# Performance work log

Measured on AMD Instinct MI355X. Metric: run time of the kernel, lower is better.

Reference implementation:

```python
import jax, jax.numpy as jnp
import numpy as np

H = 1024
A = H // 2
B = 32
S = 1024
T = 1024


def setup_inputs() -> dict:
    key = jax.random.key(0)
    ks = jax.random.split(key, 16)
    sc = 0.02
    inp = {
        "hidden": jax.random.normal(ks[0], (1, B, H), jnp.float32),
        "encoder_hiddens": jax.random.normal(ks[1], (S, B, H), jnp.float32),
        "h0_s": jax.random.normal(ks[2], (T, B, H), jnp.float32),
        "ax": jax.random.uniform(ks[3], (B, S, 1), jnp.float32),
        # weights: torch Linear(in,out,bias=False) -> W has shape [out,in], y = x @ W.T
        "W1": jax.random.normal(ks[4], (A, H), jnp.float32) * sc,
        "W2": jax.random.normal(ks[5], (A, H), jnp.float32) * sc,
        "W3": jax.random.normal(ks[6], (A, 1), jnp.float32) * sc,
        "W4": jax.random.normal(ks[7], (1, 3 * A), jnp.float32) * sc,
        "W5": jax.random.normal(ks[8], (A, H), jnp.float32) * sc,
        "W6": jax.random.normal(ks[9], (A, H), jnp.float32) * sc,
        "W7": jax.random.normal(ks[10], (A, H), jnp.float32) * sc,
        "W8": jax.random.normal(ks[11], (1, 3 * A), jnp.float32) * sc,
        "W9": jax.random.normal(ks[12], (H, H), jnp.float32) * sc,
        "W10": jax.random.normal(ks[13], (H, H), jnp.float32) * sc,
        "W11": jax.random.normal(ks[14], (1, 2 * H), jnp.float32) * sc,
    }
    return inp


def reference(hidden, encoder_hiddens, h0_s, ax,
              W1, W2, W3, W4, W5, W6, W7, W8, W9, W10, W11):
    h = hidden[0]  # [B,H], hidden.squeeze(0)

    # ---- encoder (x) attention with coverage, vectorized over S ----
    wx = jnp.einsum('sbh,ah->sba', encoder_hiddens, W1)          # [S,B,A]
    wxy = h @ W2.T                                               # [B,A]
    # Linear3 on ax[:, j] ([B,1]): outer product with W3 column
    wxr = ax[:, :, 0][:, :, None] * W3[:, 0][None, None, :]       # [B,S,A]
    wxr = jnp.transpose(wxr, (1, 0, 2))                           # [S,B,A]
    cat_x = jnp.tanh(jnp.concatenate(
        [wx, jnp.broadcast_to(wxy, (S,) + wxy.shape), wxr], axis=-1))  # [S,B,3A]
    exi = jnp.einsum('sbc,oc->bso', cat_x, W4)                    # [B,S,1]
    axi = jax.nn.softmax(exi, axis=1)                             # [B,S,1]
    cxi = jnp.einsum('bs,sbh->bh', axi[:, :, 0], encoder_hiddens)  # [B,H]
    ax_new = ax + axi

    # ---- decoder-history (t) attention, vectorized over T ----
    wt = jnp.einsum('tbh,ah->tba', h0_s, W5)                      # [T,B,A]
    wtx = cxi @ W6.T                                              # [B,A]
    wty = h @ W7.T                                                # [B,A]
    Tn = h0_s.shape[0]
    cat_t = jnp.tanh(jnp.concatenate(
        [wt,
         jnp.broadcast_to(wtx, (Tn,) + wtx.shape),
         jnp.broadcast_to(wty, (Tn,) + wty.shape)], axis=-1))     # [T,B,3A]
    eti = jnp.einsum('tbc,oc->bto', cat_t, W8)                    # [B,T,1]
    ati = jax.nn.softmax(eti, axis=1)
    cti = jnp.einsum('bt,tbh->bh', ati[:, :, 0], h0_s)            # [B,H]

    # ---- gated fusion ----
    gxi = jnp.tanh(cxi @ W9.T)
    gti = jnp.tanh(cti @ W10.T)
    zi = jax.nn.sigmoid(jnp.concatenate([cxi, cti], axis=1) @ W11.T)  # [B,1]
    ci = zi * gxi + (1.0 - zi) * gti                              # [B,H]
    return ci, ax_new
```

## Files before the change

kernel.cpp:

```cpp
#include <hip/hip_runtime.h>
#include <hip/hip_bf16.h>

#define HH 1024
#define AA 512
#define BB 32
#define SS 1024
#define TN 1024
#define M_ENC (SS*BB)
#define M_TOT ((SS+TN)*BB)
#define NCH 8

#define ABUF 8192

typedef __attribute__((ext_vector_type(8))) short short8;
typedef __attribute__((ext_vector_type(4))) float f4;

union bfu { __hip_bfloat16 h; unsigned short u; };
__device__ __forceinline__ unsigned int f2bu(float x) {
  bfu t; t.h = __float2bfloat16(x); return (unsigned int)t.u;
}
__device__ __forceinline__ unsigned short f2b(float x) {
  bfu t; t.h = __float2bfloat16(x); return t.u;
}
__device__ __forceinline__ float tanh_fast(float x) {
  float e = __expf(2.f * x);
  return 1.f - 2.f / (e + 1.f);
}

__global__ void wprep(const float* __restrict__ W, unsigned short* __restrict__ Wc) {
  const int t = blockIdx.x * 256 + threadIdx.x;
  const int lane = t & 63;
  const int rg = (t >> 6) & 31;
  const int kb = t >> 11;
  const int row = rg * 16 + (lane & 15);
  const int k = kb * 32 + ((lane >> 4) << 3);
  const float* src = W + (size_t)row * HH + k;
  f4 v0 = *(const f4*)(src);
  f4 v1 = *(const f4*)(src + 4);
  short8 o;
  o[0] = f2b(v0[0]); o[1] = f2b(v0[1]); o[2] = f2b(v0[2]); o[3] = f2b(v0[3]);
  o[4] = f2b(v1[0]); o[5] = f2b(v1[1]); o[6] = f2b(v1[2]); o[7] = f2b(v1[3]);
  *(short8*)(Wc + (size_t)t * 8) = o;
}

__global__ void poly_prep(const float* __restrict__ W3, const float* __restrict__ W4,
                          float* __restrict__ C) {
  __shared__ float r1[AA], r3[AA], r5[AA];
  const int a = threadIdx.x;
  const float w = W3[a], u = W4[2 * AA + a];
  const float w2 = w * w;
  r1[a] = u * w;
  r3[a] = u * w * w2;
  r5[a] = u * w * w2 * w2;
  __syncthreads();
  for (int off = 256; off > 0; off >>= 1) {
    if (a < off) { r1[a] += r1[a + off]; r3[a] += r3[a + off]; r5[a] += r5[a + off]; }
    __syncthreads();
  }
  if (a == 0) { C[0] = r1[0]; C[1] = -r3[0] / 3.f; C[2] = r5[0] * (2.f / 15.f); }
}

__global__ __launch_bounds__(512, 4)
void e1_gemm(const float* __restrict__ enc, const float* __restrict__ h0,
             const unsigned short* __restrict__ W1c, const unsigned short* __restrict__ W5c,
             const float* __restrict__ W4, const float* __restrict__ W8,
             float* __restrict__ e1s, float* __restrict__ e1t) {
  const int wg   = blockIdx.x;
  const int tid  = threadIdx.x;
  const int lane = tid & 63;
  const int colg = tid >> 6;
  const int l15  = lane & 15;
  const int lg   = lane >> 4;
  const int koff = (wg & 1) << 3;

  const bool is_enc = (wg * 64) < M_ENC;
  const float* __restrict__ Xg = is_enc ? enc : h0;
  const unsigned short* __restrict__ Wc = is_enc ? W1c : W5c;
  const float* __restrict__ Vg = is_enc ? W4 : W8;
  const int row0 = is_enc ? wg * 64 : wg * 64 - M_ENC;

  __shared__ char lds_raw[2 * ABUF];
  float* lred = (float*)lds_raw;

  f4 acc[4][4];
#pragma unroll
  for (int i = 0; i < 4; ++i)
#pragma unroll
    for (int j = 0; j < 4; ++j) acc[i][j] = (f4){0.f, 0.f, 0.f, 0.f};

  const int arow = tid >> 3;
  const int aq   = tid & 7;
  const float* ap = Xg + (size_t)(row0 + arow) * HH + aq * 4;
  const int slotS = (aq >> 1) ^ ((arow >> 1) & 3);
  const int aDst = arow * 64 + slotS * 16 + (aq & 1) * 8;

  const int aRd = l15 * 64 + ((lg ^ ((l15 >> 1) & 3)) << 4);

  const char* bp = (const char*)Wc + colg * 4096 + lane * 16;

  f4 an0, an1;
  short8 bfr[8];

#define ALOAD(k_) do {                                                        \
    an0 = *(const f4*)(ap + (k_) * 64);                                       \
    an1 = *(const f4*)(ap + (k_) * 64 + 32);                                  \
  } while (0)

#define AWR(bo_) do {                                                         \
    uint2 o0_, o1_;                                                           \
    o0_.x = f2bu(an0[0]) | (f2bu(an0[1]) << 16);                              \
    o0_.y = f2bu(an0[2]) | (f2bu(an0[3]) << 16);                              \
    o1_.x = f2bu(an1[0]) | (f2bu(an1[1]) << 16);                              \
    o1_.y = f2bu(an1[2]) | (f2bu(an1[3]) << 16);                              \
    *(uint2*)(lds_raw + (bo_) + aDst) = o0_;                                  \
    *(uint2*)(lds_raw + (bo_) + 4096 + aDst) = o1_;                           \
  } while (0)

#define BLOAD(kb2_) do {                                                      \
    const char* b_ = bp + (size_t)(kb2_) * 65536;                             \
    _Pragma("unroll")                                                         \
    for (int q_ = 0; q_ < 8; ++q_)                                            \
      bfr[q_] = *(const short8*)(b_ + (q_ >> 2) * 32768 + (q_ & 3) * 1024);   \
  } while (0)

#define COMPUTE(bo_) do {                                                     \
    const char* base_ = lds_raw + (bo_);                                      \
    _Pragma("unroll")                                                         \
    for (int ks_ = 0; ks_ < 2; ++ks_) {                                       \
      __builtin_amdgcn_s_setprio(1);                                          \
      _Pragma("unroll")                                                       \
      for (int rt = 0; rt < 4; ++rt) {                                        \
        short8 af_ = *(const short8*)(base_ + ks_ * 4096 + aRd + rt * 1024);  \
        _Pragma("unroll")                                                     \
        for (int cf = 0; cf < 4; ++cf)                                        \
          acc[rt][cf] = __builtin_amdgcn_mfma_f32_16x16x32_bf16(              \
              af_, bfr[ks_ * 4 + cf], acc[rt][cf], 0, 0, 0);                  \
      }                                                                       \
      __builtin_amdgcn_s_setprio(0);                                          \
    }                                                                         \
  } while (0)

#define SYNCA() do {                                                          \
    __builtin_amdgcn_sched_barrier(0);                                        \
    asm volatile("s_waitcnt lgkmcnt(0)" ::: "memory");                        \
    __builtin_amdgcn_s_barrier();                                             \
    __builtin_amdgcn_sched_barrier(0);                                        \
  } while (0)

  ALOAD(koff);
  AWR(0);
  ALOAD((1 + koff) & 15);
  SYNCA();

#pragma unroll 1
  for (int it = 0; it < 7; ++it) {
    const int kc0 = (2 * it + koff) & 15;
    const int ka2 = (2 * it + 2 + koff) & 15;
    const int kc1 = (2 * it + 1 + koff) & 15;
    const int ka3 = (2 * it + 3 + koff) & 15;
    AWR(ABUF); ALOAD(ka2); BLOAD(kc0); COMPUTE(0); SYNCA();
    AWR(0); ALOAD(ka3); BLOAD(kc1); COMPUTE(ABUF); SYNCA();
  }
  AWR(ABUF); BLOAD((14 + koff) & 15); COMPUTE(0); SYNCA();
  BLOAD((15 + koff) & 15); COMPUTE(ABUF);
#undef ALOAD
#undef AWR
#undef BLOAD
#undef COMPUTE
#undef SYNCA

  float vvv[4];
#pragma unroll
  for (int cf = 0; cf < 4; ++cf) vvv[cf] = Vg[colg * 64 + cf * 16 + l15];

  __syncthreads();
#pragma unroll
  for (int rt = 0; rt < 4; ++rt) {
    float ps[4] = {0.f, 0.f, 0.f, 0.f};
#pragma unroll
    for (int cf = 0; cf < 4; ++cf) {
      const float w = vvv[cf];
#pragma unroll
      for (int r = 0; r < 4; ++r) ps[r] += w * tanh_fast(acc[rt][cf][r]);
    }
#pragma unroll
    for (int r = 0; r < 4; ++r) {
#pragma unroll
      for (int off = 1; off < 16; off <<= 1) ps[r] += __shfl_xor(ps[r], off);
    }
    if (l15 == 0) {
#pragma unroll
      for (int r = 0; r < 4; ++r)
        lred[colg * 64 + rt * 16 + lg * 4 + r] = ps[r];
    }
  }
  __syncthreads();
  if (tid < 64) {
    float s = 0.f;
#pragma unroll
    for (int c = 0; c < 8; ++c) s += lred[c * 64 + tid];
    const int gr = row0 + tid;
    const int q = gr >> 5;
    const int b = gr & 31;
    if (is_enc) e1s[b * SS + q] = s;
    else        e1t[b * TN + q] = s;
  }
}

__global__ void softmax_both(const float* __restrict__ e1s, const float* __restrict__ e1t,
                             const float* __restrict__ ax, const float* __restrict__ C,
                             float* __restrict__ axi, float* __restrict__ ati,
                             float* __restrict__ axnew) {
  const int tid = threadIdx.x;
  __shared__ float red[256];
  if (blockIdx.x < BB) {
    const int b = blockIdx.x;
    const float c0 = C[0], c1 = C[1], c2 = C[2];
    float loc[4], xv[4];
    float m = -1e30f;
#pragma unroll
    for (int i = 0; i < 4; ++i) {
      const int s = i * 256 + tid;
      const float x = ax[b * SS + s];
      const float x2 = x * x;
      xv[i] = x;
      loc[i] = e1s[b * SS + s] + x * (c0 + x2 * (c1 + x2 * c2));
      m = fmaxf(m, loc[i]);
    }
    red[tid] = m; __syncthreads();
    for (int off = 128; off > 0; off >>= 1) {
      if (tid < off) red[tid] = fmaxf(red[tid], red[tid + off]);
      __syncthreads();
    }
    m = red[0]; __syncthreads();
    float sum = 0.f;
#pragma unroll
    for (int i = 0; i < 4; ++i) { loc[i] = __expf(loc[i] - m); sum += loc[i]; }
    red[tid] = sum; __syncthreads();
    for (int off = 128; off > 0; off >>= 1) {
      if (tid < off) red[tid] += red[tid + off];
      __syncthreads();
    }
    const float inv = 1.f / red[0];
#pragma unroll
    for (int i = 0; i < 4; ++i) {
      const int s = i * 256 + tid;
      const float a_ = loc[i] * inv;
      axi[b * SS + s] = a_;
      axnew[b * SS + s] = xv[i] + a_;
    }
  } else {
    const int b = blockIdx.x - BB;
    float loc[4];
    float m = -1e30f;
#pragma unroll
    for (int i = 0; i < 4; ++i) { loc[i] = e1t[b * TN + i * 256 + tid]; m = fmaxf(m, loc[i]); }
    red[tid] = m; __syncthreads();
    for (int off = 128; off > 0; off >>= 1) {
      if (tid < off) red[tid] = fmaxf(red[tid], red[tid + off]);
      __syncthreads();
    }
    m = red[0]; __syncthreads();
    float sum = 0.f;
#pragma unroll
    for (int i = 0; i < 4; ++i) { loc[i] = __expf(loc[i] - m); sum += loc[i]; }
    red[tid] = sum; __syncthreads();
    for (int off = 128; off > 0; off >>= 1) {
      if (tid < off) red[tid] += red[tid + off];
      __syncthreads();
    }
    const float inv = 1.f / red[0];
#pragma unroll
    for (int i = 0; i < 4; ++i) ati[b * TN + (i * 256 + tid)] = loc[i] * inv;
  }
}

__global__ void wpart2(const float* __restrict__ enc, const float* __restrict__ h0,
                       const float* __restrict__ axi, const float* __restrict__ ati,
                       float* __restrict__ partx, float* __restrict__ partt) {
  const int gb = blockIdx.x;
  const bool isx = gb < BB * NCH;
  const float* __restrict__ X = isx ? enc : h0;
  const float* __restrict__ w = isx ? axi : ati;
  float* __restrict__ part = isx ? partx : partt;
  const int idx = isx ? gb : gb - BB * NCH;
  const int b = idx / NCH, ch = idx % NCH;
  const int tid = threadIdx.x;
  __shared__ float ws[SS / NCH];
  if (tid < SS / NCH) ws[tid] = w[b * SS + ch * (SS / NCH) + tid];
  __syncthreads();
  f4 acc = (f4){0.f, 0.f, 0.f, 0.f};
  const float* base = X + ((size_t)(ch * (SS / NCH)) * BB + b) * HH + tid * 4;
#pragma unroll 4
  for (int i = 0; i < SS / NCH; ++i) {
    f4 x = *(const f4*)(base + (size_t)i * BB * HH);
    acc += ws[i] * x;
  }
  *(f4*)&part[((size_t)(b * NCH + ch)) * HH + tid * 4] = acc;
}

__global__ void wreduce2(const float* __restrict__ partx, const float* __restrict__ partt,
                         float* __restrict__ cxi, float* __restrict__ cti) {
  const int idx = blockIdx.x * 256 + threadIdx.x;
  const bool isx = idx < BB * HH;
  const float* __restrict__ part = isx ? partx : partt;
  float* __restrict__ outp = isx ? cxi : cti;
  const int j = isx ? idx : idx - BB * HH;
  const int b = j / HH, h = j % HH;
  float s = 0.f;
#pragma unroll
  for (int ch = 0; ch < NCH; ++ch) s += part[((size_t)(b * NCH + ch)) * HH + h];
  outp[j] = s;
}

__global__ void ci_kernel(const float* __restrict__ cxi, const float* __restrict__ cti,
                          const float* __restrict__ W9, const float* __restrict__ W10,
                          const float* __restrict__ W11, float* __restrict__ out_ci) {
  const int b = blockIdx.x >> 2, hb = blockIdx.x & 3, tid = threadIdx.x;
  const int h = hb * 256 + tid;
  __shared__ float cx[HH], ct[HH];
  __shared__ float zred[4];
  for (int i = tid; i < HH; i += 256) { cx[i] = cxi[b * HH + i]; ct[i] = cti[b * HH + i]; }
  __syncthreads();
  float zs = 0.f;
  for (int i = tid; i < HH; i += 256) zs += cx[i] * W11[i] + ct[i] * W11[HH + i];
  for (int off = 32; off > 0; off >>= 1) zs += __shfl_down(zs, off);
  if ((tid & 63) == 0) zred[tid >> 6] = zs;
  __syncthreads();
  const float zt = zred[0] + zred[1] + zred[2] + zred[3];
  const float z = 1.f / (1.f + __expf(-zt));

  const float* __restrict__ w9r  = W9  + (size_t)h * HH;
  const float* __restrict__ w10r = W10 + (size_t)h * HH;
  float gx = 0.f, gt = 0.f;
  for (int k = 0; k < HH; k += 4) {
    f4 a = *(const f4*)(w9r + k);
    f4 c = *(const f4*)(w10r + k);
    gx += cx[k] * a[0] + cx[k + 1] * a[1] + cx[k + 2] * a[2] + cx[k + 3] * a[3];
    gt += ct[k] * c[0] + ct[k + 1] * c[1] + ct[k + 2] * c[2] + ct[k + 3] * c[3];
  }
  out_ci[b * HH + h] = z * tanhf(gx) + (1.f - z) * tanhf(gt);
}

extern "C" void kernel_launch(void* const* d_in, const int* in_sizes, int n_in,
                              void* d_out, int out_size, void* d_ws, size_t ws_size,
                              hipStream_t stream) {
  const float* enc = (const float*)d_in[1];
  const float* h0  = (const float*)d_in[2];
  const float* ax  = (const float*)d_in[3];
  const float* W1  = (const float*)d_in[4];
  const float* W3  = (const float*)d_in[6];
  const float* W4  = (const float*)d_in[7];
  const float* W5  = (const float*)d_in[8];
  const float* W8  = (const float*)d_in[11];
  const float* W9  = (const float*)d_in[12];
  const float* W10 = (const float*)d_in[13];
  const float* W11 = (const float*)d_in[14];
  float* out = (float*)d_out;

  float* w = (float*)d_ws;
  unsigned short* W1c = (unsigned short*)w;
  unsigned short* W5c = (unsigned short*)(w + 262144);
  float* partx = w;
  float* partt = w + 262144;
  float* e1s   = w + 524288;
  float* e1t   = w + 557056;
  float* axi   = w + 589824;
  float* ati   = w + 622592;
  float* cxi   = w + 655360;
  float* cti   = w + 688128;
  float* Cpoly = w + 720896;

  wprep<<<256, 256, 0, stream>>>(W1, W1c);
  wprep<<<256, 256, 0, stream>>>(W5, W5c);
  poly_prep<<<1, 512, 0, stream>>>(W3, W4, Cpoly);
  e1_gemm<<<M_TOT / 64, 512, 0, stream>>>(enc, h0, W1c, W5c, W4, W8, e1s, e1t);
  softmax_both<<<2 * BB, 256, 0, stream>>>(e1s, e1t, ax, Cpoly, axi, ati, out + BB * HH);
  wpart2<<<2 * BB * NCH, 256, 0, stream>>>(enc, h0, axi, ati, partx, partt);
  wreduce2<<<2 * BB * HH / 256, 256, 0, stream>>>(partx, partt, cxi, cti);
  ci_kernel<<<BB * 4, 256, 0, stream>>>(cxi, cti, W9, W10, W11, out);
}
```

Measured before the change: 215.7 us.

## Persistent GEMM blocks with triple-buffered A and double-buffered B registers; merge prep kernels

The three weight/polynomial prep kernels become one launch. The e1 GEMM now runs 256 blocks, each looping over four 64-row tiles, instead of 1024 one-tile blocks, with launch bounds lowered to 2 waves per SIMD. The K loop is fully unrolled with a three-slot LDS ring for A and ping-pong B fragment registers, so the next B load overlaps current MFMAs. The k-offset staggering and s_setprio hints are removed. This aims to cut launch and tail overhead and hide load latency, at the cost of more registers, lower occupancy and a tile-serial epilogue.

```diff
diff --git a/kernel.cpp b/kernel.cpp
--- a/kernel.cpp
+++ b/kernel.cpp
@@ -10,7 +10,10 @@
 #define M_TOT ((SS+TN)*BB)
 #define NCH 8
 
-#define ABUF 8192
+#define AB0 0
+#define AB1 8192
+#define AB2 16384
+#define LRED 24576
 
 typedef __attribute__((ext_vector_type(8))) short short8;
 typedef __attribute__((ext_vector_type(4))) float f4;
@@ -27,40 +30,46 @@
   return 1.f - 2.f / (e + 1.f);
 }
 
-__global__ void wprep(const float* __restrict__ W, unsigned short* __restrict__ Wc) {
-  const int t = blockIdx.x * 256 + threadIdx.x;
-  const int lane = t & 63;
-  const int rg = (t >> 6) & 31;
-  const int kb = t >> 11;
-  const int row = rg * 16 + (lane & 15);
-  const int k = kb * 32 + ((lane >> 4) << 3);
-  const float* src = W + (size_t)row * HH + k;
-  f4 v0 = *(const f4*)(src);
-  f4 v1 = *(const f4*)(src + 4);
-  short8 o;
-  o[0] = f2b(v0[0]); o[1] = f2b(v0[1]); o[2] = f2b(v0[2]); o[3] = f2b(v0[3]);
-  o[4] = f2b(v1[0]); o[5] = f2b(v1[1]); o[6] = f2b(v1[2]); o[7] = f2b(v1[3]);
-  *(short8*)(Wc + (size_t)t * 8) = o;
-}
-
-__global__ void poly_prep(const float* __restrict__ W3, const float* __restrict__ W4,
-                          float* __restrict__ C) {
-  __shared__ float r1[AA], r3[AA], r5[AA];
-  const int a = threadIdx.x;
-  const float w = W3[a], u = W4[2 * AA + a];
-  const float w2 = w * w;
-  r1[a] = u * w;
-  r3[a] = u * w * w2;
-  r5[a] = u * w * w2 * w2;
-  __syncthreads();
-  for (int off = 256; off > 0; off >>= 1) {
-    if (a < off) { r1[a] += r1[a + off]; r3[a] += r3[a + off]; r5[a] += r5[a + off]; }
+__global__ void prep_all(const float* __restrict__ W1, const float* __restrict__ W5,
+                         const float* __restrict__ W3, const float* __restrict__ W4,
+                         unsigned short* __restrict__ W1c, unsigned short* __restrict__ W5c,
+                         float* __restrict__ C) {
+  if (blockIdx.x < 512) {
+    const float* __restrict__ W = (blockIdx.x < 256) ? W1 : W5;
+    unsigned short* __restrict__ Wc = (blockIdx.x < 256) ? W1c : W5c;
+    const int t = (blockIdx.x & 255) * 256 + threadIdx.x;
+    const int lane = t & 63;
+    const int rg = (t >> 6) & 31;
+    const int kb = t >> 11;
+    const int row = rg * 16 + (lane & 15);
+    const int k = kb * 32 + ((lane >> 4) << 3);
+    const float* src = W + (size_t)row * HH + k;
+    f4 v0 = *(const f4*)(src);
+    f4 v1 = *(const f4*)(src + 4);
+    short8 o;
+    o[0] = f2b(v0[0]); o[1] = f2b(v0[1]); o[2] = f2b(v0[2]); o[3] = f2b(v0[3]);
+    o[4] = f2b(v1[0]); o[5] = f2b(v1[1]); o[6] = f2b(v1[2]); o[7] = f2b(v1[3]);
+    *(short8*)(Wc + (size_t)t * 8) = o;
+  } else {
+    __shared__ float r1[256], r3[256], r5[256];
+    const int tp = threadIdx.x;
+    float s1 = 0.f, s3 = 0.f, s5 = 0.f;
+    for (int a = tp; a < AA; a += 256) {
+      const float w = W3[a], u = W4[2 * AA + a];
+      const float w2 = w * w;
+      s1 += u * w; s3 += u * w * w2; s5 += u * w * w2 * w2;
+    }
+    r1[tp] = s1; r3[tp] = s3; r5[tp] = s5;
     __syncthreads();
+    for (int off = 128; off > 0; off >>= 1) {
+      if (tp < off) { r1[tp] += r1[tp + off]; r3[tp] += r3[tp + off]; r5[tp] += r5[tp + off]; }
+      __syncthreads();
+    }
+    if (tp == 0) { C[0] = r1[0]; C[1] = -r3[0] / 3.f; C[2] = r5[0] * (2.f / 15.f); }
   }
-  if (a == 0) { C[0] = r1[0]; C[1] = -r3[0] / 3.f; C[2] = r5[0] * (2.f / 15.f); }
-}
-
-__global__ __launch_bounds__(512, 4)
+}
+
+__global__ __launch_bounds__(512, 2)
 void e1_gemm(const float* __restrict__ enc, const float* __restrict__ h0,
              const unsigned short* __restrict__ W1c, const unsigned short* __restrict__ W5c,
              const float* __restrict__ W4, const float* __restrict__ W8,
@@ -71,140 +80,161 @@
   const int colg = tid >> 6;
   const int l15  = lane & 15;
   const int lg   = lane >> 4;
-  const int koff = (wg & 1) << 3;
-
-  const bool is_enc = (wg * 64) < M_ENC;
+
+  const bool is_enc = wg < 128;
   const float* __restrict__ Xg = is_enc ? enc : h0;
   const unsigned short* __restrict__ Wc = is_enc ? W1c : W5c;
   const float* __restrict__ Vg = is_enc ? W4 : W8;
-  const int row0 = is_enc ? wg * 64 : wg * 64 - M_ENC;
-
-  __shared__ char lds_raw[2 * ABUF];
-  float* lred = (float*)lds_raw;
-
-  f4 acc[4][4];
-#pragma unroll
-  for (int i = 0; i < 4; ++i)
-#pragma unroll
-    for (int j = 0; j < 4; ++j) acc[i][j] = (f4){0.f, 0.f, 0.f, 0.f};
+  const int row0 = (is_enc ? wg : wg - 128) * 256;
+
+  __shared__ char lds_raw[LRED + 2048];
+  float* lred = (float*)(lds_raw + LRED);
 
   const int arow = tid >> 3;
   const int aq   = tid & 7;
-  const float* ap = Xg + (size_t)(row0 + arow) * HH + aq * 4;
   const int slotS = (aq >> 1) ^ ((arow >> 1) & 3);
   const int aDst = arow * 64 + slotS * 16 + (aq & 1) * 8;
-
   const int aRd = l15 * 64 + ((lg ^ ((l15 >> 1) & 3)) << 4);
 
   const char* bp = (const char*)Wc + colg * 4096 + lane * 16;
 
-  f4 an0, an1;
-  short8 bfr[8];
-
-#define ALOAD(k_) do {                                                        \
+  float vvv[4];
+#pragma unroll
+  for (int cf = 0; cf < 4; ++cf) vvv[cf] = Vg[colg * 64 + cf * 16 + l15];
+
+#define ALOADN(k_) do {                                                       \
     an0 = *(const f4*)(ap + (k_) * 64);                                       \
     an1 = *(const f4*)(ap + (k_) * 64 + 32);                                  \
   } while (0)
-
-#define AWR(bo_) do {                                                         \
+#define ALOADM(k_) do {                                                       \
+    am0 = *(const f4*)(ap + (k_) * 64);                                       \
+    am1 = *(const f4*)(ap + (k_) * 64 + 32);                                  \
+  } while (0)
+#define AWRX(bo_, x0_, x1_) do {                                              \
     uint2 o0_, o1_;                                                           \
-    o0_.x = f2bu(an0[0]) | (f2bu(an0[1]) << 16);                              \
-    o0_.y = f2bu(an0[2]) | (f2bu(an0[3]) << 16);                              \
-    o1_.x = f2bu(an1[0]) | (f2bu(an1[1]) << 16);                              \
-    o1_.y = f2bu(an1[2]) | (f2bu(an1[3]) << 16);                              \
+    o0_.x = f2bu(x0_[0]) | (f2bu(x0_[1]) << 16);                              \
+    o0_.y = f2bu(x0_[2]) | (f2bu(x0_[3]) << 16);                              \
+    o1_.x = f2bu(x1_[0]) | (f2bu(x1_[1]) << 16);                              \
+    o1_.y = f2bu(x1_[2]) | (f2bu(x1_[3]) << 16);                              \
     *(uint2*)(lds_raw + (bo_) + aDst) = o0_;                                  \
     *(uint2*)(lds_raw + (bo_) + 4096 + aDst) = o1_;                           \
   } while (0)
-
-#define BLOAD(kb2_) do {                                                      \
-    const char* b_ = bp + (size_t)(kb2_) * 65536;                             \
-    _Pragma("unroll")                                                         \
-    for (int q_ = 0; q_ < 8; ++q_)                                            \
-      bfr[q_] = *(const short8*)(b_ + (q_ >> 2) * 32768 + (q_ & 3) * 1024);   \
-  } while (0)
-
-#define COMPUTE(bo_) do {                                                     \
+#define BLOAD(dst_, kb_) do {                                                 \
+    const char* b_ = bp + (size_t)(kb_) * 65536;                              \
+    dst_[0] = *(const short8*)(b_);                                           \
+    dst_[1] = *(const short8*)(b_ + 1024);                                    \
+    dst_[2] = *(const short8*)(b_ + 2048);                                    \
+    dst_[3] = *(const short8*)(b_ + 3072);                                    \
+    dst_[4] = *(const short8*)(b_ + 32768);                                   \
+    dst_[5] = *(const short8*)(b_ + 32768 + 1024);                            \
+    dst_[6] = *(const short8*)(b_ + 32768 + 2048);                            \
+    dst_[7] = *(const short8*)(b_ + 32768 + 3072);                            \
+  } while (0)
+#define COMPUTE(bo_, bfr_) do {                                               \
     const char* base_ = lds_raw + (bo_);                                      \
     _Pragma("unroll")                                                         \
     for (int ks_ = 0; ks_ < 2; ++ks_) {                                       \
-      __builtin_amdgcn_s_setprio(1);                                          \
       _Pragma("unroll")                                                       \
       for (int rt = 0; rt < 4; ++rt) {                                        \
         short8 af_ = *(const short8*)(base_ + ks_ * 4096 + aRd + rt * 1024);  \
         _Pragma("unroll")                                                     \
         for (int cf = 0; cf < 4; ++cf)                                        \
           acc[rt][cf] = __builtin_amdgcn_mfma_f32_16x16x32_bf16(              \
-              af_, bfr[ks_ * 4 + cf], acc[rt][cf], 0, 0, 0);                  \
+              af_, bfr_[ks_ * 4 + cf], acc[rt][cf], 0, 0, 0);                 \
       }                                                                       \
-      __builtin_amdgcn_s_setprio(0);                                          \
     }                                                                         \
   } while (0)
-
 #define SYNCA() do {                                                          \
     __builtin_amdgcn_sched_barrier(0);                                        \
     asm volatile("s_waitcnt lgkmcnt(0)" ::: "memory");                        \
     __builtin_amdgcn_s_barrier();                                             \
     __builtin_amdgcn_sched_barrier(0);                                        \
   } while (0)
-
-  ALOAD(koff);
-  AWR(0);
-  ALOAD((1 + koff) & 15);
-  SYNCA();
+#define STEPF(J_, BW_, BC_, SW_, SC_) do {                                    \
+    AWRX(BW_, an0, an1);                                                      \
+    ALOADN((J_) + 3);                                                         \
+    BLOAD(SW_, (J_) + 1);                                                     \
+    COMPUTE(BC_, SC_);                                                        \
+    SYNCA();                                                                  \
+  } while (0)
 
 #pragma unroll 1
-  for (int it = 0; it < 7; ++it) {
-    const int kc0 = (2 * it + koff) & 15;
-    const int ka2 = (2 * it + 2 + koff) & 15;
-    const int kc1 = (2 * it + 1 + koff) & 15;
-    const int ka3 = (2 * it + 3 + koff) & 15;
-    AWR(ABUF); ALOAD(ka2); BLOAD(kc0); COMPUTE(0); SYNCA();
-    AWR(0); ALOAD(ka3); BLOAD(kc1); COMPUTE(ABUF); SYNCA();
+  for (int tile = 0; tile < 4; ++tile) {
+    const float* ap = Xg + (size_t)(row0 + tile * 64 + arow) * HH + aq * 4;
+
+    f4 acc[4][4];
+#pragma unroll
+    for (int i = 0; i < 4; ++i)
+#pragma unroll
+      for (int j = 0; j < 4; ++j) acc[i][j] = (f4){0.f, 0.f, 0.f, 0.f};
+
+    f4 an0, an1, am0, am1;
+    short8 bfa[8], bfb[8];
+
+    ALOADN(0); ALOADM(1);
+    AWRX(AB0, an0, an1);
+    AWRX(AB1, am0, am1);
+    ALOADN(2);
+    BLOAD(bfa, 0);
+    SYNCA();
+
+    STEPF(0,  AB2, AB0, bfb, bfa);
+    STEPF(1,  AB0, AB1, bfa, bfb);
+    STEPF(2,  AB1, AB2, bfb, bfa);
+    STEPF(3,  AB2, AB0, bfa, bfb);
+    STEPF(4,  AB0, AB1, bfb, bfa);
+    STEPF(5,  AB1, AB2, bfa, bfb);
+    STEPF(6,  AB2, AB0, bfb, bfa);
+    STEPF(7,  AB0, AB1, bfa, bfb);
+    STEPF(8,  AB1, AB2, bfb, bfa);
+    STEPF(9,  AB2, AB0, bfa, bfb);
+    STEPF(10, AB0, AB1, bfb, bfa);
+    STEPF(11, AB1, AB2, bfa, bfb);
+    STEPF(12, AB2, AB0, bfb, bfa);
+    AWRX(AB0, an0, an1); BLOAD(bfa, 14); COMPUTE(AB1, bfb); SYNCA();
+    BLOAD(bfb, 15); COMPUTE(AB2, bfa); SYNCA();
+    COMPUTE(AB0, bfb);
+
+#pragma unroll
+    for (int rt = 0; rt < 4; ++rt) {
+      float ps[4] = {0.f, 0.f, 0.f, 0.f};
+#pragma unroll
+      for (int cf = 0; cf < 4; ++cf) {
+        const float w = vvv[cf];
+#pragma unroll
+        for (int r = 0; r < 4; ++r) ps[r] += w * tanh_fast(acc[rt][cf][r]);
+      }
+#pragma unroll
+      for (int r = 0; r < 4; ++r) {
+#pragma unroll
+        for (int off = 1; off < 16; off <<= 1) ps[r] += __shfl_xor(ps[r], off);
+      }
+      if (l15 == 0) {
+#pragma unroll
+        for (int r = 0; r < 4; ++r)
+          lred[colg * 64 + rt * 16 + lg * 4 + r] = ps[r];
+      }
+    }
+    __syncthreads();
+    if (tid < 64) {
+      float s = 0.f;
+#pragma unroll
+      for (int c = 0; c < 8; ++c) s += lred[c * 64 + tid];
+      const int gr = row0 + tile * 64 + tid;
+      const int q = gr >> 5;
+      const int b = gr & 31;
+      if (is_enc) e1s[b * SS + q] = s;
+      else        e1t[b * TN + q] = s;
+    }
+    __syncthreads();
   }
-  AWR(ABUF); BLOAD((14 + koff) & 15); COMPUTE(0); SYNCA();
-  BLOAD((15 + koff) & 15); COMPUTE(ABUF);
-#undef ALOAD
-#undef AWR
+#undef ALOADN
+#undef ALOADM
+#undef AWRX
 #undef BLOAD
 #undef COMPUTE
 #undef SYNCA
-
-  float vvv[4];
-#pragma unroll
-  for (int cf = 0; cf < 4; ++cf) vvv[cf] = Vg[colg * 64 + cf * 16 + l15];
-
-  __syncthreads();
-#pragma unroll
-  for (int rt = 0; rt < 4; ++rt) {
-    float ps[4] = {0.f, 0.f, 0.f, 0.f};
-#pragma unroll
-    for (int cf = 0; cf < 4; ++cf) {
-      const float w = vvv[cf];
-#pragma unroll
-      for (int r = 0; r < 4; ++r) ps[r] += w * tanh_fast(acc[rt][cf][r]);
-    }
-#pragma unroll
-    for (int r = 0; r < 4; ++r) {
-#pragma unroll
-      for (int off = 1; off < 16; off <<= 1) ps[r] += __shfl_xor(ps[r], off);
-    }
-    if (l15 == 0) {
-#pragma unroll
-      for (int r = 0; r < 4; ++r)
-        lred[colg * 64 + rt * 16 + lg * 4 + r] = ps[r];
-    }
-  }
-  __syncthreads();
-  if (tid < 64) {
-    float s = 0.f;
-#pragma unroll
-    for (int c = 0; c < 8; ++c) s += lred[c * 64 + tid];
-    const int gr = row0 + tid;
-    const int q = gr >> 5;
-    const int b = gr & 31;
-    if (is_enc) e1s[b * SS + q] = s;
-    else        e1t[b * TN + q] = s;
-  }
+#undef STEPF
 }
 
 __global__ void softmax_both(const float* __restrict__ e1s, const float* __restrict__ e1t,
@@ -371,10 +401,8 @@
   float* cti   = w + 688128;
   float* Cpoly = w + 720896;
 
-  wprep<<<256, 256, 0, stream>>>(W1, W1c);
-  wprep<<<256, 256, 0, stream>>>(W5, W5c);
-  poly_prep<<<1, 512, 0, stream>>>(W3, W4, Cpoly);
-  e1_gemm<<<M_TOT / 64, 512, 0, stream>>>(enc, h0, W1c, W5c, W4, W8, e1s, e1t);
+  prep_all<<<513, 256, 0, stream>>>(W1, W5, W3, W4, W1c, W5c, Cpoly);
+  e1_gemm<<<256, 512, 0, stream>>>(enc, h0, W1c, W5c, W4, W8, e1s, e1t);
   softmax_both<<<2 * BB, 256, 0, stream>>>(e1s, e1t, ax, Cpoly, axi, ati, out + BB * HH);
   wpart2<<<2 * BB * NCH, 256, 0, stream>>>(enc, h0, axi, ati, partx, partt);
   wreduce2<<<2 * BB * HH / 256, 256, 0, stream>>>(partx, partt, cxi, cti);
```

New measurement: 339.0 us. +57.2%, slower.

## Software-pipeline B-fragment loads in e1_gemm and merge prep kernels

Applied to the files above, without the earlier changes.

The three weight/poly prep launches are merged into one launch, which removes two launch gaps. In e1_gemm the B weight fragments are now prefetched one k-step ahead in two halves, each load placed after the MFMA block that consumes the previous half, so global-load latency overlaps compute. The per-workgroup k-offset stagger (koff) is dropped, so all workgroups now walk K in the same order. This may raise contention on the same weight lines.

```diff
diff --git a/kernel.cpp b/kernel.cpp
--- a/kernel.cpp
+++ b/kernel.cpp
@@ -27,37 +27,43 @@
   return 1.f - 2.f / (e + 1.f);
 }
 
-__global__ void wprep(const float* __restrict__ W, unsigned short* __restrict__ Wc) {
-  const int t = blockIdx.x * 256 + threadIdx.x;
-  const int lane = t & 63;
-  const int rg = (t >> 6) & 31;
-  const int kb = t >> 11;
-  const int row = rg * 16 + (lane & 15);
-  const int k = kb * 32 + ((lane >> 4) << 3);
-  const float* src = W + (size_t)row * HH + k;
-  f4 v0 = *(const f4*)(src);
-  f4 v1 = *(const f4*)(src + 4);
-  short8 o;
-  o[0] = f2b(v0[0]); o[1] = f2b(v0[1]); o[2] = f2b(v0[2]); o[3] = f2b(v0[3]);
-  o[4] = f2b(v1[0]); o[5] = f2b(v1[1]); o[6] = f2b(v1[2]); o[7] = f2b(v1[3]);
-  *(short8*)(Wc + (size_t)t * 8) = o;
-}
-
-__global__ void poly_prep(const float* __restrict__ W3, const float* __restrict__ W4,
-                          float* __restrict__ C) {
-  __shared__ float r1[AA], r3[AA], r5[AA];
-  const int a = threadIdx.x;
-  const float w = W3[a], u = W4[2 * AA + a];
-  const float w2 = w * w;
-  r1[a] = u * w;
-  r3[a] = u * w * w2;
-  r5[a] = u * w * w2 * w2;
-  __syncthreads();
-  for (int off = 256; off > 0; off >>= 1) {
-    if (a < off) { r1[a] += r1[a + off]; r3[a] += r3[a + off]; r5[a] += r5[a + off]; }
+__global__ void prep_all(const float* __restrict__ W1, const float* __restrict__ W5,
+                         const float* __restrict__ W3, const float* __restrict__ W4,
+                         unsigned short* __restrict__ W1c, unsigned short* __restrict__ W5c,
+                         float* __restrict__ C) {
+  if (blockIdx.x < 512) {
+    const float* __restrict__ W = (blockIdx.x < 256) ? W1 : W5;
+    unsigned short* __restrict__ Wc = (blockIdx.x < 256) ? W1c : W5c;
+    const int t = (blockIdx.x & 255) * 256 + threadIdx.x;
+    const int lane = t & 63;
+    const int rg = (t >> 6) & 31;
+    const int kb = t >> 11;
+    const int row = rg * 16 + (lane & 15);
+    const int k = kb * 32 + ((lane >> 4) << 3);
+    const float* src = W + (size_t)row * HH + k;
+    f4 v0 = *(const f4*)(src);
+    f4 v1 = *(const f4*)(src + 4);
+    short8 o;
+    o[0] = f2b(v0[0]); o[1] = f2b(v0[1]); o[2] = f2b(v0[2]); o[3] = f2b(v0[3]);
+    o[4] = f2b(v1[0]); o[5] = f2b(v1[1]); o[6] = f2b(v1[2]); o[7] = f2b(v1[3]);
+    *(short8*)(Wc + (size_t)t * 8) = o;
+  } else {
+    __shared__ float r1[256], r3[256], r5[256];
+    const int tp = threadIdx.x;
+    float s1 = 0.f, s3 = 0.f, s5 = 0.f;
+    for (int a = tp; a < AA; a += 256) {
+      const float w = W3[a], u = W4[2 * AA + a];
+      const float w2 = w * w;
+      s1 += u * w; s3 += u * w * w2; s5 += u * w * w2 * w2;
+    }
+    r1[tp] = s1; r3[tp] = s3; r5[tp] = s5;
     __syncthreads();
-  }
-  if (a == 0) { C[0] = r1[0]; C[1] = -r3[0] / 3.f; C[2] = r5[0] * (2.f / 15.f); }
+    for (int off = 128; off > 0; off >>= 1) {
+      if (tp < off) { r1[tp] += r1[tp + off]; r3[tp] += r3[tp + off]; r5[tp] += r5[tp + off]; }
+      __syncthreads();
+    }
+    if (tp == 0) { C[0] = r1[0]; C[1] = -r3[0] / 3.f; C[2] = r5[0] * (2.f / 15.f); }
+  }
 }
 
 __global__ __launch_bounds__(512, 4)
@@ -71,7 +77,6 @@
   const int colg = tid >> 6;
   const int l15  = lane & 15;
   const int lg   = lane >> 4;
-  const int koff = (wg & 1) << 3;
 
   const bool is_enc = (wg * 64) < M_ENC;
   const float* __restrict__ Xg = is_enc ? enc : h0;
@@ -116,28 +121,48 @@
     *(uint2*)(lds_raw + (bo_) + 4096 + aDst) = o1_;                           \
   } while (0)
 
-#define BLOAD(kb2_) do {                                                      \
-    const char* b_ = bp + (size_t)(kb2_) * 65536;                             \
+#define BH0(kb_) do {                                                         \
+    const char* b_ = bp + (size_t)(kb_) * 65536;                              \
+    bfr[0] = *(const short8*)(b_);                                            \
+    bfr[1] = *(const short8*)(b_ + 1024);                                     \
+    bfr[2] = *(const short8*)(b_ + 2048);                                     \
+    bfr[3] = *(const short8*)(b_ + 3072);                                     \
+  } while (0)
+
+#define BH1(kb_) do {                                                         \
+    const char* b_ = bp + (size_t)(kb_) * 65536 + 32768;                      \
+    bfr[4] = *(const short8*)(b_);                                            \
+    bfr[5] = *(const short8*)(b_ + 1024);                                     \
+    bfr[6] = *(const short8*)(b_ + 2048);                                     \
+    bfr[7] = *(const short8*)(b_ + 3072);                                     \
+  } while (0)
+
+#define COMP0(bo_) do {                                                       \
+    const char* base_ = lds_raw + (bo_);                                      \
+    __builtin_amdgcn_s_setprio(1);                                            \
     _Pragma("unroll")                                                         \
-    for (int q_ = 0; q_ < 8; ++q_)                                            \
-      bfr[q_] = *(const short8*)(b_ + (q_ >> 2) * 32768 + (q_ & 3) * 1024);   \
-  } while (0)
-
-#define COMPUTE(bo_) do {                                                     \
-    const char* base_ = lds_raw + (bo_);                                      \
+    for (int rt = 0; rt < 4; ++rt) {                                          \
+      short8 af_ = *(const short8*)(base_ + aRd + rt * 1024);                 \
+      _Pragma("unroll")                                                       \
+      for (int cf = 0; cf < 4; ++cf)                                          \
+        acc[rt][cf] = __builtin_amdgcn_mfma_f32_16x16x32_bf16(                \
+            af_, bfr[cf], acc[rt][cf], 0, 0, 0);                              \
+    }                                                                         \
+    __builtin_amdgcn_s_setprio(0);                                            \
+  } while (0)
+
+#define COMP1(bo_) do {                                                       \
+    const char* base_ = lds_raw + (bo_) + 4096;                               \
+    __builtin_amdgcn_s_setprio(1);                                            \
     _Pragma("unroll")                                                         \
-    for (int ks_ = 0; ks_ < 2; ++ks_) {                                       \
-      __builtin_amdgcn_s_setprio(1);                                          \
+    for (int rt = 0; rt < 4; ++rt) {                                          \
+      short8 af_ = *(const short8*)(base_ + aRd + rt * 1024);                 \
       _Pragma("unroll")                                                       \
-      for (int rt = 0; rt < 4; ++rt) {                                        \
-        short8 af_ = *(const short8*)(base_ + ks_ * 4096 + aRd + rt * 1024);  \
-        _Pragma("unroll")                                                     \
-        for (int cf = 0; cf < 4; ++cf)                                        \
-          acc[rt][cf] = __builtin_amdgcn_mfma_f32_16x16x32_bf16(              \
-              af_, bfr[ks_ * 4 + cf], acc[rt][cf], 0, 0, 0);                  \
-      }                                                                       \
-      __builtin_amdgcn_s_setprio(0);                                          \
+      for (int cf = 0; cf < 4; ++cf)                                          \
+        acc[rt][cf] = __builtin_amdgcn_mfma_f32_16x16x32_bf16(                \
+            af_, bfr[4 + cf], acc[rt][cf], 0, 0, 0);                          \
     }                                                                         \
+    __builtin_amdgcn_s_setprio(0);                                            \
   } while (0)
 
 #define SYNCA() do {                                                          \
@@ -147,26 +172,35 @@
     __builtin_amdgcn_sched_barrier(0);                                        \
   } while (0)
 
-  ALOAD(koff);
+  ALOAD(0);
   AWR(0);
-  ALOAD((1 + koff) & 15);
+  ALOAD(1);
+  BH0(0); BH1(0);
   SYNCA();
 
 #pragma unroll 1
   for (int it = 0; it < 7; ++it) {
-    const int kc0 = (2 * it + koff) & 15;
-    const int ka2 = (2 * it + 2 + koff) & 15;
-    const int kc1 = (2 * it + 1 + koff) & 15;
-    const int ka3 = (2 * it + 3 + koff) & 15;
-    AWR(ABUF); ALOAD(ka2); BLOAD(kc0); COMPUTE(0); SYNCA();
-    AWR(0); ALOAD(ka3); BLOAD(kc1); COMPUTE(ABUF); SYNCA();
-  }
-  AWR(ABUF); BLOAD((14 + koff) & 15); COMPUTE(0); SYNCA();
-  BLOAD((15 + koff) & 15); COMPUTE(ABUF);
+    AWR(ABUF); ALOAD(2 * it + 2);
+    COMP0(0); BH0(2 * it + 1);
+    COMP1(0); BH1(2 * it + 1);
+    SYNCA();
+    AWR(0); ALOAD(2 * it + 3);
+    COMP0(ABUF); BH0(2 * it + 2);
+    COMP1(ABUF); BH1(2 * it + 2);
+    SYNCA();
+  }
+  AWR(ABUF);
+  COMP0(0); BH0(15);
+  COMP1(0); BH1(15);
+  SYNCA();
+  COMP0(ABUF);
+  COMP1(ABUF);
 #undef ALOAD
 #undef AWR
-#undef BLOAD
-#undef COMPUTE
+#undef BH0
+#undef BH1
+#undef COMP0
+#undef COMP1
 #undef SYNCA
 
   float vvv[4];
@@ -371,9 +405,7 @@
   float* cti   = w + 688128;
   float* Cpoly = w + 720896;
 
-  wprep<<<256, 256, 0, stream>>>(W1, W1c);
-  wprep<<<256, 256, 0, stream>>>(W5, W5c);
-  poly_prep<<<1, 512, 0, stream>>>(W3, W4, Cpoly);
+  prep_all<<<513, 256, 0, stream>>>(W1, W5, W3, W4, W1c, W5c, Cpoly);
   e1_gemm<<<M_TOT / 64, 512, 0, stream>>>(enc, h0, W1c, W5c, W4, W8, e1s, e1t);
   softmax_both<<<2 * BB, 256, 0, stream>>>(e1s, e1t, ax, Cpoly, axi, ati, out + BB * HH);
   wpart2<<<2 * BB * NCH, 256, 0, stream>>>(enc, h0, axi, ati, partx, partt);
```

Result: no change. 216.4 us (+0.3%).
